# Kernel optimization log

Measured on AMD Instinct MI355X. Metric: run time of the kernel, lower is better.

The kernel has to match this reference:

```python
import math
import jax, jax.numpy as jnp
import numpy as np

NUM_HEADS = 12
ALPHA, BETA, GAMMA = 1.9, 3.8, 15.2  # get_rpe_config(ratio=1.9)
SKIP = 1


def _rp_bucket(side):
    """iRPE euclidean contextual bucket table for a side x side grid + 1 cls token."""
    beta_int = int(BETA)
    coords = np.stack(np.meshgrid(np.arange(side), np.arange(side), indexing='ij'), -1).reshape(-1, 2)
    diff = coords[:, None, :] - coords[None, :, :]
    dis = np.round(np.sqrt((diff ** 2).sum(-1).astype(np.float64)))  # rounded euclidean distance
    far = np.clip(np.round(ALPHA + np.log(np.maximum(dis, 1e-9) / ALPHA) / math.log(GAMMA / ALPHA) * (BETA - ALPHA)), None, BETA)
    idx = np.where(dis <= ALPHA, dis, far).astype(np.int32) + beta_int
    num_buckets = 2 * beta_int + 1  # 7
    L = side * side
    full = np.full((L + SKIP, L + SKIP), num_buckets, dtype=np.int32)  # extra bucket for cls
    full[SKIP:, SKIP:] = idx
    return full, num_buckets + 1  # table [P,P], total buckets = 8


def setup_inputs() -> dict:
    key = jax.random.key(0)
    ks = jax.random.split(key, 8)
    B, P, n_mod, C = 64, 197, 2, 768
    N = 1 + (P - 1) * n_mod  # 393
    hd = C // NUM_HEADS
    rp_bucket, n_buckets = _rp_bucket(int(math.sqrt(P - SKIP)))
    s = 0.02
    return {
        'x': jax.random.normal(ks[0], (B, N, C), jnp.float32),
        'q_learned': jax.random.normal(ks[1], (1, 1, C), jnp.float32) * s,
        'pos_embed': jax.random.normal(ks[2], (1, P, C), jnp.float32) * s,
        'wk': jax.random.normal(ks[3], (C, C), jnp.float32) * s,
        'wv': jax.random.normal(ks[4], (C, C), jnp.float32) * s,
        'rpe_w': jax.random.normal(ks[5], (hd, n_buckets), jnp.float32) * s,  # shared_head ctx lookup table
        'proj_w': jax.random.normal(ks[6], (C, C), jnp.float32) * s,
        'proj_b': jnp.zeros((C,), jnp.float32),
        'rp_bucket': jnp.asarray(rp_bucket),  # [P, P] int32
    }


def reference(x, q_learned, pos_embed, wk, wv, rpe_w, proj_w, proj_b, rp_bucket):
    B, N, C = x.shape
    H = NUM_HEADS
    hd = C // H
    P = rp_bucket.shape[0]
    n_mod = (N - 1) // (P - 1)
    scale = hd ** -0.5

    q_ = jnp.broadcast_to(q_learned + pos_embed, (B, P, C))
    q = q_.reshape(B, P, H, hd).transpose(0, 2, 1, 3)                    # bhpd
    k = (x @ wk.T).reshape(B, N, H, hd).transpose(0, 2, 1, 3)            # bhnd
    v = (x @ wv.T).reshape(B, N, H, hd).transpose(0, 2, 1, 3)            # bhnd

    attn = jnp.einsum('bhpd,bhnd->bhpn', q, k) * scale                   # [B,H,P,N]

    # contextual RPE on keys: lookup = q @ table, gathered by rp_bucket[i, j]
    lookup = jnp.einsum('bhpd,du->bhpu', q, rpe_w)                        # [B,H,P,n_buckets]
    bias = lookup[:, :, jnp.arange(P)[:, None], rp_bucket]                # [B,H,P,P]
    bias = jnp.concatenate([bias[..., :1], jnp.tile(bias[..., 1:], (1, 1, 1, n_mod))], axis=-1)
    attn = jax.nn.softmax(attn + bias, axis=-1)

    out = jnp.einsum('bhpn,bhnd->bhpd', attn, v).transpose(0, 2, 1, 3).reshape(B, P, C)
    return out @ proj_w.T + proj_b
```

## Files before the change

### kernel.cpp

```cpp
#include <hip/hip_runtime.h>

typedef unsigned short u16;
typedef short bf16x8 __attribute__((ext_vector_type(8)));
typedef float f32x4 __attribute__((ext_vector_type(4)));
typedef const __attribute__((address_space(1))) void* gptr_t;
typedef __attribute__((address_space(3))) void* lptr_t;

#define B_   64
#define N_   393
#define C_   768
#define H_   12
#define HD_  64
#define P_   197
#define BIAS_N 416
#define PPAD 208
#define VTP  448
#define M_KV (B_ * N_)
#define M_PR (B_ * P_)
#define SCALE_L2E 0.180336879f

__device__ __forceinline__ u16 f2bf(float f) {
    unsigned u = __float_as_uint(f);
    return (u16)((u + 0x7FFFu + ((u >> 16) & 1u)) >> 16);
}
__device__ __forceinline__ unsigned cvt_pk_bf16(float lo, float hi) {
    unsigned r;
    asm("v_cvt_pk_bf16_f32 %0, %1, %2" : "=v"(r) : "v"(lo), "v"(hi));
    return r;
}
__device__ __forceinline__ float exp2_fast(float x) {
    float r;
    asm("v_exp_f32 %0, %1" : "=v"(r) : "v"(x));
    return r;
}

__global__ __launch_bounds__(256) void f2bf_kernel(const float* __restrict__ in,
                                                   u16* __restrict__ out, int n4) {
    int i = blockIdx.x * 256 + threadIdx.x;
    if (i < n4) {
        float4 v = ((const float4*)in)[i];
        u16 o[4] = {f2bf(v.x), f2bf(v.y), f2bf(v.z), f2bf(v.w)};
        *(uint2*)(out + i * 4) = *(uint2*)o;
    }
}

__global__ __launch_bounds__(256) void convw_kernel(
    const float* __restrict__ wk, const float* __restrict__ wv,
    const float* __restrict__ pw, u16* __restrict__ wkvh, u16* __restrict__ pwh) {
    int sec = blockIdx.x / 576;
    int i = (blockIdx.x % 576) * 256 + threadIdx.x;
    const float* src = sec == 0 ? wk : (sec == 1 ? wv : pw);
    u16* dst = sec == 0 ? wkvh : (sec == 1 ? wkvh + 589824 : pwh);
    float4 v = ((const float4*)src)[i];
    u16 o[4] = {f2bf(v.x), f2bf(v.y), f2bf(v.z), f2bf(v.w)};
    *(uint2*)(dst + i * 4) = *(uint2*)o;
}

__global__ __launch_bounds__(256) void prep1_kernel(
    const float* __restrict__ q_learned, const float* __restrict__ pos_embed,
    const float* __restrict__ rpe_w, u16* __restrict__ qh, float* __restrict__ lk)
{
    __shared__ float q_s[C_];
    const int p = blockIdx.x, t = threadIdx.x;
    for (int c = t; c < C_; c += 256) {
        float v = q_learned[c] + pos_embed[p * C_ + c];
        q_s[c] = v;
        qh[p * C_ + c] = f2bf(v);
    }
    __syncthreads();
    if (t < H_ * 8) {
        int h = t >> 3, u = t & 7;
        float s = 0.f;
        #pragma unroll 8
        for (int d = 0; d < HD_; ++d)
            s = fmaf(q_s[h * HD_ + d], rpe_w[d * 8 + u], s);
        lk[(h * P_ + p) * 8 + u] = s;
    }
}

__global__ __launch_bounds__(256) void prep2_kernel(
    const float* __restrict__ lk, const int* __restrict__ rp_bucket,
    float* __restrict__ biasT)
{
    int bx = blockIdx.x;
    int h = bx / N_, j = bx % N_;
    int t = threadIdx.x;
    if (t >= PPAD) return;
    int jm;
    if (j == 0) jm = 0;
    else { jm = j - 1; if (jm >= 196) jm -= 196; jm += 1; }
    float v = 0.f;
    if (t < P_) {
        int bucket = rp_bucket[t * P_ + jm];
        v = lk[(h * P_ + t) * 8 + bucket] * 1.44269504f;
    }
    biasT[((size_t)h * BIAS_N + j) * PPAD + t] = v;
}

template <bool F32OUT>
__global__ __launch_bounds__(256) void gemm_bf16(
    const u16* __restrict__ A, const u16* __restrict__ Bw,
    u16* __restrict__ Cb, float* __restrict__ Cf, const float* __restrict__ bias,
    int M, int ldc)
{
    __shared__ __align__(16) u16 As[128 * 64];
    __shared__ __align__(16) u16 Bs[128 * 64];

    const int gx = gridDim.x;
    const int nwg = gx * gridDim.y;
    const int orig = blockIdx.y * gx + blockIdx.x;
    const int xcd = orig & 7, rank = orig >> 3;
    const int q = nwg >> 3, r = nwg & 7;
    const int wgid = (xcd < r ? xcd * (q + 1) : r * (q + 1) + (xcd - r) * q) + rank;
    const int n0 = (wgid % gx) * 128;
    const int m0 = (wgid / gx) * 128;

    const int t = threadIdx.x;
    const int w = t >> 6, l = t & 63;
    const int wr = w >> 1, wc = w & 1;
    const int l15 = l & 15, lg = l >> 4;
    const int lrow = l >> 3, lslot = l & 7;
    const int Mc = M - 1;

    f32x4 acc[4][4];
    #pragma unroll
    for (int i = 0; i < 4; ++i)
        #pragma unroll
        for (int j = 0; j < 4; ++j) acc[i][j] = (f32x4){0.f, 0.f, 0.f, 0.f};

    for (int ks = 0; ks < 12; ++ks) {
        const int k0 = ks * 64;
        if (ks) __syncthreads();
        #pragma unroll
        for (int i = 0; i < 4; ++i) {
            const int rbase = w * 32 + i * 8;
            int arow = m0 + rbase + lrow; if (arow > Mc) arow = Mc;
            const int brow = n0 + rbase + lrow;
            const u16* ga = A  + (size_t)arow * 768 + k0 + lslot * 8;
            const u16* gb = Bw + (size_t)brow * 768 + k0 + lslot * 8;
            __builtin_amdgcn_global_load_lds((gptr_t)(const void*)ga,
                                             (lptr_t)(void*)(As + rbase * 64), 16, 0, 0);
            __builtin_amdgcn_global_load_lds((gptr_t)(const void*)gb,
                                             (lptr_t)(void*)(Bs + rbase * 64), 16, 0, 0);
        }
        __syncthreads();
        #pragma unroll
        for (int kk = 0; kk < 2; ++kk) {
            bf16x8 af[4], bfr[4];
            #pragma unroll
            for (int mf = 0; mf < 4; ++mf) {
                af[mf]  = *(const bf16x8*)(As + (wr * 64 + mf * 16 + l15) * 64 + (kk * 4 + lg) * 8);
                bfr[mf] = *(const bf16x8*)(Bs + (wc * 64 + mf * 16 + l15) * 64 + (kk * 4 + lg) * 8);
            }
            #pragma unroll
            for (int mf = 0; mf < 4; ++mf)
                #pragma unroll
                for (int nf = 0; nf < 4; ++nf)
                    acc[mf][nf] = __builtin_amdgcn_mfma_f32_16x16x32_bf16(
                        af[mf], bfr[nf], acc[mf][nf], 0, 0, 0);
        }
    }

    #pragma unroll
    for (int mf = 0; mf < 4; ++mf) {
        #pragma unroll
        for (int nf = 0; nf < 4; ++nf) {
            int col = n0 + wc * 64 + nf * 16 + l15;
            float bb = 0.f;
            if (F32OUT) bb = bias[col];
            #pragma unroll
            for (int rr = 0; rr < 4; ++rr) {
                int m = m0 + wr * 64 + mf * 16 + lg * 4 + rr;
                if (m < M) {
                    if (F32OUT) Cf[(size_t)m * ldc + col] = acc[mf][nf][rr] + bb;
                    else        Cb[(size_t)m * ldc + col] = f2bf(acc[mf][nf][rr]);
                }
            }
        }
    }
}

__global__ __launch_bounds__(256) void vtrans_kernel(const u16* __restrict__ KV,
                                                     u16* __restrict__ Vt)
{
    const int bh = blockIdx.x;
    const int b = bh / H_, h = bh % H_;
    const int t = threadIdx.x, w = t >> 6, l = t & 63;
    const int d = w * 16 + (l >> 2);
    const int c = l & 3;
    const u16* src = KV + (size_t)b * N_ * 1536 + 768 + h * HD_ + d;
    u16* dst = Vt + (size_t)(bh * HD_ + d) * VTP;
    for (int jb = 0; jb < VTP; jb += 32) {
        int j0 = jb + c * 8;
        u16 v[8];
        #pragma unroll
        for (int i = 0; i < 8; ++i) {
            int j = j0 + i;
            v[i] = (j < N_) ? src[(size_t)j * 1536] : (u16)0;
        }
        *(bf16x8*)(dst + j0) = *(bf16x8*)v;
    }
}

__global__ __launch_bounds__(256, 2) void attn_mfma3(
    const u16* __restrict__ qh, const u16* __restrict__ KV,
    const u16* __restrict__ Vt, const float* __restrict__ biasT,
    u16* __restrict__ Obuf)
{
    __shared__ __align__(16) u16 pts[64 * 456];
    __shared__ __align__(16) u16 kvs[2][64 * 64];

    const int id = blockIdx.x;
    const int work = (id & 7) * 384 + (id >> 3);
    const int ptile = work & 3;
    const int rest = work >> 2;
    const int h = rest % 12;
    const int b = rest / 12;
    const int p0 = ptile * 64;

    const int t = threadIdx.x, w = t >> 6, l = t & 63;
    const int l15 = l & 15, lg = l >> 4;
    const int p0w = p0 + w * 16;

    int srow[2], sslot[2], swoff[2];
    #pragma unroll
    for (int i = 0; i < 2; ++i) {
        int c = t + 256 * i;
        srow[i] = c >> 3; sslot[i] = c & 7;
        swoff[i] = srow[i] * 64 + ((sslot[i] ^ (srow[i] & 7)) << 3);
    }

    int prow = p0w + l15; if (prow > P_ - 1) prow = P_ - 1;
    const u16* qp = qh + (size_t)prow * C_ + h * HD_ + lg * 8;
    bf16x8 qf0 = *(const bf16x8*)(qp);
    bf16x8 qf1 = *(const bf16x8*)(qp + 32);

    const u16* Kbase = KV + (size_t)b * (N_ * 1536) + h * HD_;
    const u16* Vbase = Vt + (size_t)(b * H_ + h) * (HD_ * VTP);

    f32x4 acc[7][4];
    #pragma unroll
    for (int i = 0; i < 7; ++i)
        #pragma unroll
        for (int j = 0; j < 4; ++j) acc[i][j] = (f32x4){0.f, 0.f, 0.f, 0.f};

    bf16x8 ra[2];
    #pragma unroll
    for (int i = 0; i < 2; ++i)
        ra[i] = *(const bf16x8*)(Kbase + (size_t)srow[i] * 1536 + sslot[i] * 8);
    #pragma unroll
    for (int i = 0; i < 2; ++i) *(bf16x8*)(&kvs[0][swoff[i]]) = ra[i];
    __syncthreads();

    #pragma unroll
    for (int nt = 0; nt < 7; ++nt) {
        const u16* kcur = kvs[nt & 1];
        if (nt < 6) {
            #pragma unroll
            for (int i = 0; i < 2; ++i) {
                int rn = (nt + 1) * 64 + srow[i]; if (rn > N_ - 1) rn = N_ - 1;
                ra[i] = *(const bf16x8*)(Kbase + (size_t)rn * 1536 + sslot[i] * 8);
            }
        }
        __builtin_amdgcn_s_setprio(1);
        #pragma unroll
        for (int kc = 0; kc < 2; ++kc)
            #pragma unroll
            for (int sub = 0; sub < 4; ++sub) {
                int row = sub * 16 + l15;
                bf16x8 kb = *(const bf16x8*)(kcur + row * 64 + (((kc * 4 + lg) ^ (row & 7)) << 3));
                acc[nt][sub] = __builtin_amdgcn_mfma_f32_16x16x32_bf16(
                    kc ? qf1 : qf0, kb, acc[nt][sub], 0, 0, 0);
            }
        __builtin_amdgcn_s_setprio(0);
        if (nt < 6) {
            #pragma unroll
            for (int i = 0; i < 2; ++i) *(bf16x8*)(&kvs[(nt + 1) & 1][swoff[i]]) = ra[i];
        }
        __syncthreads();
    }

    #pragma unroll
    for (int i = 0; i < 2; ++i)
        ra[i] = *(const bf16x8*)(Vbase + (size_t)srow[i] * VTP + sslot[i] * 8);

    const int pcl = (p0w + lg * 4) > (PPAD - 4) ? (PPAD - 4) : (p0w + lg * 4);
    float s4[4] = {0.f, 0.f, 0.f, 0.f};
    #pragma unroll
    for (int nt = 0; nt < 7; ++nt)
        #pragma unroll
        for (int sub = 0; sub < 4; ++sub) {
            int n = nt * 64 + sub * 16 + l15;
            if (n < N_) {
                float4 b4 = *(const float4*)(biasT + ((size_t)h * BIAS_N + n) * PPAD + pcl);
                float bb[4] = {b4.x, b4.y, b4.z, b4.w};
                #pragma unroll
                for (int rr = 0; rr < 4; ++rr) {
                    float e = exp2_fast(fmaf(acc[nt][sub][rr], SCALE_L2E, bb[rr]));
                    acc[nt][sub][rr] = e;
                    s4[rr] += e;
                }
            } else {
                acc[nt][sub] = (f32x4){0.f, 0.f, 0.f, 0.f};
            }
        }
    float rinv4[4];
    #pragma unroll
    for (int rr = 0; rr < 4; ++rr) {
        float s = s4[rr];
        s += __shfl_xor(s, 1); s += __shfl_xor(s, 2);
        s += __shfl_xor(s, 4); s += __shfl_xor(s, 8);
        rinv4[rr] = 1.0f / s;
    }

    {
        const int rowb = w * 16 + lg * 4;
        #pragma unroll
        for (int nt = 0; nt < 7; ++nt)
            #pragma unroll
            for (int sub = 0; sub < 4; ++sub) {
                int col = nt * 64 + sub * 16 + l15;
                unsigned pk01 = cvt_pk_bf16(acc[nt][sub][0] * rinv4[0],
                                            acc[nt][sub][1] * rinv4[1]);
                unsigned pk23 = cvt_pk_bf16(acc[nt][sub][2] * rinv4[2],
                                            acc[nt][sub][3] * rinv4[3]);
                pts[(rowb + 0) * 456 + col] = (u16)pk01;
                pts[(rowb + 1) * 456 + col] = (u16)(pk01 >> 16);
                pts[(rowb + 2) * 456 + col] = (u16)pk23;
                pts[(rowb + 3) * 456 + col] = (u16)(pk23 >> 16);
            }
    }
    #pragma unroll
    for (int i = 0; i < 2; ++i) *(bf16x8*)(&kvs[0][swoff[i]]) = ra[i];
    __syncthreads();

    f32x4 o[4];
    #pragma unroll
    for (int i = 0; i < 4; ++i) o[i] = (f32x4){0.f, 0.f, 0.f, 0.f};

    #pragma unroll
    for (int nt = 0; nt < 7; ++nt) {
        const u16* kcur = kvs[nt & 1];
        if (nt < 6) {
            #pragma unroll
            for (int i = 0; i < 2; ++i)
                ra[i] = *(const bf16x8*)(Vbase + (size_t)srow[i] * VTP + (nt + 1) * 64 + sslot[i] * 8);
        }
        __builtin_amdgcn_s_setprio(1);
        #pragma unroll
        for (int kc = 0; kc < 2; ++kc) {
            bf16x8 pa = *(const bf16x8*)(pts + (w * 16 + l15) * 456 + nt * 64 + kc * 32 + lg * 8);
            #pragma unroll
            for (int dsub = 0; dsub < 4; ++dsub) {
                int row = dsub * 16 + l15;
                bf16x8 vb = *(const bf16x8*)(kcur + row * 64 + (((kc * 4 + lg) ^ (row & 7)) << 3));
                o[dsub] = __builtin_amdgcn_mfma_f32_16x16x32_bf16(pa, vb, o[dsub], 0, 0, 0);
            }
        }
        __builtin_amdgcn_s_setprio(0);
        if (nt < 6) {
            #pragma unroll
            for (int i = 0; i < 2; ++i) *(bf16x8*)(&kvs[(nt + 1) & 1][swoff[i]]) = ra[i];
        }
        __syncthreads();
    }

    #pragma unroll
    for (int dsub = 0; dsub < 4; ++dsub)
        #pragma unroll
        for (int rr = 0; rr < 4; ++rr) {
            int p = p0w + lg * 4 + rr;
            if (p < P_)
                Obuf[((size_t)b * P_ + p) * C_ + h * HD_ + dsub * 16 + l15] = f2bf(o[dsub][rr]);
        }
}

extern "C" void kernel_launch(void* const* d_in, const int* in_sizes, int n_in,
                              void* d_out, int out_size, void* d_ws, size_t ws_size,
                              hipStream_t stream)
{
    const float* x         = (const float*)d_in[0];
    const float* q_learned = (const float*)d_in[1];
    const float* pos_embed = (const float*)d_in[2];
    const float* wk        = (const float*)d_in[3];
    const float* wv        = (const float*)d_in[4];
    const float* rpe_w     = (const float*)d_in[5];
    const float* proj_w    = (const float*)d_in[6];
    const float* proj_b    = (const float*)d_in[7];
    const int*   rp_bucket = (const int*)d_in[8];
    float* out = (float*)d_out;

    char* ws = (char*)d_ws;
    u16*   xh    = (u16*)(ws);
    u16*   wkvh  = (u16*)(ws + 38633472);
    u16*   pwh   = (u16*)(ws + 40992768);
    u16*   qh    = (u16*)(ws + 42172416);
    float* lk    = (float*)(ws + 42475008);
    float* biasT = (float*)(ws + 42550784);
    u16*   KV    = (u16*)(ws + 46704128);
    u16*   Vt    = (u16*)(ws + 123971072);
    u16*   Obuf  = (u16*)(ws + 168011264);

    f2bf_kernel<<<(19316736 / 4 + 255) / 256, 256, 0, stream>>>(x, xh, 19316736 / 4);
    convw_kernel<<<3 * 576, 256, 0, stream>>>(wk, wv, proj_w, wkvh, pwh);

    prep1_kernel<<<P_, 256, 0, stream>>>(q_learned, pos_embed, rpe_w, qh, lk);
    prep2_kernel<<<H_ * N_, 256, 0, stream>>>(lk, rp_bucket, biasT);

    dim3 gkv(1536 / 128, (M_KV + 127) / 128);
    gemm_bf16<false><<<gkv, 256, 0, stream>>>(xh, wkvh, KV, nullptr, nullptr, M_KV, 1536);

    vtrans_kernel<<<B_ * H_, 256, 0, stream>>>(KV, Vt);

    attn_mfma3<<<3072, 256, 0, stream>>>(qh, KV, Vt, biasT, Obuf);

    dim3 gpr(768 / 128, (M_PR + 127) / 128);
    gemm_bf16<true><<<gpr, 256, 0, stream>>>(Obuf, pwh, nullptr, out, proj_b, M_PR, 768);
}
```

Baseline: 242.5 us.

## Double-buffer GEMM LDS tiles with XOR swizzle and MFMA priority boost

```diff
diff --git a/kernel.cpp b/kernel.cpp
--- a/kernel.cpp
+++ b/kernel.cpp
@@ -103,8 +103,8 @@
     u16* __restrict__ Cb, float* __restrict__ Cf, const float* __restrict__ bias,
     int M, int ldc)
 {
-    __shared__ __align__(16) u16 As[128 * 64];
-    __shared__ __align__(16) u16 Bs[128 * 64];
+    __shared__ __align__(16) u16 As[2][128 * 64];
+    __shared__ __align__(16) u16 Bs[2][128 * 64];
 
     const int gx = gridDim.x;
     const int nwg = gx * gridDim.y;
@@ -119,46 +119,81 @@
     const int w = t >> 6, l = t & 63;
     const int wr = w >> 1, wc = w & 1;
     const int l15 = l & 15, lg = l >> 4;
-    const int lrow = l >> 3, lslot = l & 7;
     const int Mc = M - 1;
 
+    int srow[4], sssrc[4];
+    const u16* gAb[4];
+    const u16* gBb[4];
+    #pragma unroll
+    for (int i = 0; i < 4; ++i) {
+        int c = t + 256 * i;
+        int row = c >> 3, s = c & 7;
+        int ssrc = s ^ (row & 7);
+        srow[i] = row; sssrc[i] = ssrc;
+        int arow = m0 + row; if (arow > Mc) arow = Mc;
+        gAb[i] = A + (size_t)arow * 768 + ssrc * 8;
+        gBb[i] = Bw + (size_t)(n0 + row) * 768 + ssrc * 8;
+    }
+
+    int aoff[4][2], boff[4][2];
+    #pragma unroll
+    for (int mf = 0; mf < 4; ++mf)
+        #pragma unroll
+        for (int kk = 0; kk < 2; ++kk) {
+            int row = wr * 64 + mf * 16 + l15;
+            int s = kk * 4 + lg;
+            aoff[mf][kk] = row * 64 + ((s ^ (row & 7)) << 3);
+            row = wc * 64 + mf * 16 + l15;
+            boff[mf][kk] = row * 64 + ((s ^ (row & 7)) << 3);
+        }
+
     f32x4 acc[4][4];
     #pragma unroll
     for (int i = 0; i < 4; ++i)
         #pragma unroll
         for (int j = 0; j < 4; ++j) acc[i][j] = (f32x4){0.f, 0.f, 0.f, 0.f};
 
+    #pragma unroll
+    for (int i = 0; i < 4; ++i) {
+        int c = t + 256 * i;
+        __builtin_amdgcn_global_load_lds((gptr_t)(const void*)(gAb[i]),
+                                         (lptr_t)(void*)(&As[0][c * 8]), 16, 0, 0);
+        __builtin_amdgcn_global_load_lds((gptr_t)(const void*)(gBb[i]),
+                                         (lptr_t)(void*)(&Bs[0][c * 8]), 16, 0, 0);
+    }
+    __syncthreads();
+
     for (int ks = 0; ks < 12; ++ks) {
-        const int k0 = ks * 64;
-        if (ks) __syncthreads();
-        #pragma unroll
-        for (int i = 0; i < 4; ++i) {
-            const int rbase = w * 32 + i * 8;
-            int arow = m0 + rbase + lrow; if (arow > Mc) arow = Mc;
-            const int brow = n0 + rbase + lrow;
-            const u16* ga = A  + (size_t)arow * 768 + k0 + lslot * 8;
-            const u16* gb = Bw + (size_t)brow * 768 + k0 + lslot * 8;
-            __builtin_amdgcn_global_load_lds((gptr_t)(const void*)ga,
-                                             (lptr_t)(void*)(As + rbase * 64), 16, 0, 0);
-            __builtin_amdgcn_global_load_lds((gptr_t)(const void*)gb,
-                                             (lptr_t)(void*)(Bs + rbase * 64), 16, 0, 0);
-        }
-        __syncthreads();
+        const int d = ks & 1;
+        if (ks < 11) {
+            const int k0n = (ks + 1) * 64;
+            #pragma unroll
+            for (int i = 0; i < 4; ++i) {
+                int c = t + 256 * i;
+                __builtin_amdgcn_global_load_lds((gptr_t)(const void*)(gAb[i] + k0n),
+                                                 (lptr_t)(void*)(&As[d ^ 1][c * 8]), 16, 0, 0);
+                __builtin_amdgcn_global_load_lds((gptr_t)(const void*)(gBb[i] + k0n),
+                                                 (lptr_t)(void*)(&Bs[d ^ 1][c * 8]), 16, 0, 0);
+            }
+        }
         #pragma unroll
         for (int kk = 0; kk < 2; ++kk) {
             bf16x8 af[4], bfr[4];
             #pragma unroll
             for (int mf = 0; mf < 4; ++mf) {
-                af[mf]  = *(const bf16x8*)(As + (wr * 64 + mf * 16 + l15) * 64 + (kk * 4 + lg) * 8);
-                bfr[mf] = *(const bf16x8*)(Bs + (wc * 64 + mf * 16 + l15) * 64 + (kk * 4 + lg) * 8);
-            }
+                af[mf]  = *(const bf16x8*)(&As[d][aoff[mf][kk]]);
+                bfr[mf] = *(const bf16x8*)(&Bs[d][boff[mf][kk]]);
+            }
+            __builtin_amdgcn_s_setprio(1);
             #pragma unroll
             for (int mf = 0; mf < 4; ++mf)
                 #pragma unroll
                 for (int nf = 0; nf < 4; ++nf)
                     acc[mf][nf] = __builtin_amdgcn_mfma_f32_16x16x32_bf16(
                         af[mf], bfr[nf], acc[mf][nf], 0, 0, 0);
-        }
+            __builtin_amdgcn_s_setprio(0);
+        }
+        __syncthreads();
     }
 
     #pragma unroll
```

Measured after the change: 257.9 us. 6.3% more time.
